# Kernel optimization log

Hardware: AMD Instinct MI355X
Metric: run time of the kernel (lower is better)

Reference implementation:

```python
import jax, jax.numpy as jnp
import numpy as np

N_USERS = 150000
N_ENTITIES = 250000
CH = 64
N_REL = 17
N_FACTORS = 4
N_EDGES = 1_000_000
NNZ = 1_000_000
N_HOPS = 2


def setup_inputs() -> dict:
    key = jax.random.key(0)
    ks = jax.random.split(key, 10)
    user_emb = jax.random.normal(ks[0], (N_USERS, CH), jnp.float32) * 0.1
    entity_emb = jax.random.normal(ks[1], (N_ENTITIES, CH), jnp.float32) * 0.1
    latent_emb = jax.random.normal(ks[2], (N_FACTORS, CH), jnp.float32) * 0.1
    weight = jax.random.normal(ks[3], (N_REL - 1, CH), jnp.float32) * 0.1
    disen_weight_att = jax.random.normal(ks[4], (N_FACTORS, N_REL - 1), jnp.float32) * 0.1
    edge_index = jax.random.randint(ks[5], (2, N_EDGES), 0, N_ENTITIES)
    edge_type = jax.random.randint(ks[6], (N_EDGES,), 1, N_REL)  # in [1, N_REL-1]
    inter_row = jax.random.randint(ks[7], (NNZ,), 0, N_USERS)
    inter_col = jax.random.randint(ks[8], (NNZ,), 0, N_ENTITIES)
    inter_val = jax.random.uniform(ks[9], (NNZ,), jnp.float32)
    return {
        "user_emb": user_emb, "entity_emb": entity_emb, "latent_emb": latent_emb,
        "weight": weight, "disen_weight_att": disen_weight_att, "inter_val": inter_val,
        "edge_index": edge_index, "edge_type": edge_type,
        "inter_row": inter_row, "inter_col": inter_col,
    }


def _l2norm(x):
    # F.normalize(x, dim=1) with eps=1e-12
    n = jnp.linalg.norm(x, axis=1, keepdims=True)
    return x / jnp.maximum(n, 1e-12)


def reference(user_emb, entity_emb, latent_emb, weight, disen_weight_att,
              inter_val, edge_index, edge_type, inter_row, inter_col):
    n_entities = entity_emb.shape[0]
    n_users = user_emb.shape[0]
    head, tail = edge_index[0], edge_index[1]

    # _cul_cor with ind='cosine': sum_{i<j} cos(w_i, w_j)^2 over rows of disen_weight_att
    wn = disen_weight_att / jnp.linalg.norm(disen_weight_att, axis=1, keepdims=True)
    gram = (wn @ wn.T) ** 2  # [F, F]
    cor = jnp.sum(jnp.triu(gram, k=1))

    # constants across hops
    counts = jax.ops.segment_sum(jnp.ones(head.shape[0], jnp.float32), head,
                                 num_segments=n_entities)
    denom = jnp.maximum(counts, 1.0)[:, None]  # scatter_mean denominator (0 -> keep 0)
    disen_weight = jax.nn.softmax(disen_weight_att, axis=-1) @ weight  # [F, C]

    e, u = entity_emb, user_emb
    ent_res, usr_res = entity_emb, user_emb
    for _ in range(N_HOPS):
        # KG aggregate: per-edge gather, relation modulation, scatter_mean into heads
        neigh = e[tail] * weight[edge_type - 1]              # [E, C]
        entity_agg = jax.ops.segment_sum(neigh, head, num_segments=n_entities) / denom

        # user -> latent factor attention
        score = jax.nn.softmax(u @ latent_emb.T, axis=1)[:, :, None]  # [U, F, 1]

        # user aggregate: sparse interact_mat @ entity_emb
        user_agg = jax.ops.segment_sum(inter_val[:, None] * e[inter_col], inter_row,
                                       num_segments=n_users)  # [U, C]
        mix = jnp.sum(disen_weight[None, :, :] * score, axis=1)  # [U, C]
        user_agg = user_agg * mix + user_agg

        e = _l2norm(entity_agg)
        u = _l2norm(user_agg)
        ent_res = ent_res + e
        usr_res = usr_res + u
    return ent_res, usr_res, cor
```

## Files before the change

### kernel.cpp

```cpp
#include <hip/hip_runtime.h>
#include <hip/hip_bf16.h>

#define N_USERS    150000
#define N_ENTITIES 250000
#define CHN        64
#define N_RELM1    16
#define N_FACTORS  4
#define N_EDGES    1000000
#define NNZ_       1000000
#define NRECS      (N_EDGES + NNZ_)

#define BROWS      1024
#define RCAP       8192
#define RCAP_OUT   8192
#define EBUCKETS   245
#define USR0       (EBUCKETS * BROWS)
#define ROWS_EFF   (USR0 + N_USERS)
#define NB         392
#define TILE_A     4096
#define TA_THREADS 512
#define ITEMS_A    8

typedef float vf4 __attribute__((ext_vector_type(4)));

__device__ __forceinline__ unsigned short f2bf(float f) {
    unsigned u = __float_as_uint(f);
    return (unsigned short)((u + 0x7fffu + ((u >> 16) & 1u)) >> 16);
}

__global__ __launch_bounds__(512) void prep_small_kernel(const float* __restrict__ weight,
                                  const float* __restrict__ att,
                                  float* __restrict__ disenw,
                                  float* __restrict__ cor_out,
                                  int* __restrict__ bcur)
{
    int tid = threadIdx.x;
    if (tid < NB) bcur[tid] = tid * RCAP;

    if (tid < 256) {
        int f  = tid >> 6;
        int ch = tid & 63;
        float m = -1e30f;
        for (int r = 0; r < N_RELM1; ++r) m = fmaxf(m, att[f * N_RELM1 + r]);
        float ex[N_RELM1];
        float s = 0.f;
        for (int r = 0; r < N_RELM1; ++r) { ex[r] = expf(att[f * N_RELM1 + r] - m); s += ex[r]; }
        float inv = 1.f / s;
        float acc = 0.f;
        for (int r = 0; r < N_RELM1; ++r) acc += (ex[r] * inv) * weight[r * CHN + ch];
        disenw[f * CHN + ch] = acc;
    }

    if (tid == 0) {
        float wn[N_FACTORS][N_RELM1];
        for (int i = 0; i < N_FACTORS; ++i) {
            float ss = 0.f;
            for (int r = 0; r < N_RELM1; ++r) { float v = att[i * N_RELM1 + r]; ss += v * v; }
            float innv = 1.f / sqrtf(ss);
            for (int r = 0; r < N_RELM1; ++r) wn[i][r] = att[i * N_RELM1 + r] * innv;
        }
        float cor = 0.f;
        for (int i = 0; i < N_FACTORS; ++i)
            for (int j = i + 1; j < N_FACTORS; ++j) {
                float d = 0.f;
                for (int r = 0; r < N_RELM1; ++r) d += wn[i][r] * wn[j][r];
                cor += d * d;
            }
        cor_out[0] = cor;
    }
}

__global__ __launch_bounds__(256) void conv_bf16_kernel(const float4* __restrict__ src,
                                                        ushort4* __restrict__ dst, int n4)
{
    int i = blockIdx.x * 256 + threadIdx.x;
    if (i >= n4) return;
    float4 v = src[i];
    dst[i] = make_ushort4(f2bf(v.x), f2bf(v.y), f2bf(v.z), f2bf(v.w));
}

__global__ __launch_bounds__(TA_THREADS) void bin_pass_kernel(
    const int* __restrict__ head, const int* __restrict__ tail,
    const int* __restrict__ etype, const int* __restrict__ irow,
    const int* __restrict__ icol, const float* __restrict__ val,
    int* __restrict__ bcur, unsigned long long* __restrict__ binned)
{
    __shared__ int cntS[NB], startS[NB], gbase[NB];
    __shared__ unsigned long long buf[TILE_A];
    __shared__ unsigned short bk[TILE_A];

    int tid = threadIdx.x;
    if (tid < NB) cntS[tid] = 0;
    __syncthreads();

    int base = blockIdx.x * TILE_A;
    unsigned long long p[ITEMS_A];
    int bkt[ITEMS_A], rnk[ITEMS_A];
    #pragma unroll
    for (int j = 0; j < ITEMS_A; ++j) {
        int i = base + j * TA_THREADS + tid;
        bkt[j] = -1;
        if (i < NRECS) {
            int row; unsigned long long pay;
            if (i < N_EDGES) {
                row = head[i];
                pay = ((unsigned long long)(unsigned)(etype[i] - 1) << 18) | (unsigned)tail[i];
            } else {
                int jj = i - N_EDGES;
                row = USR0 + irow[jj];
                pay = ((unsigned long long)__float_as_uint(val[jj]) << 18) | (unsigned)icol[jj];
            }
            p[j] = pay | ((unsigned long long)(unsigned)(row & (BROWS - 1)) << 50);
            bkt[j] = row >> 10;
            rnk[j] = atomicAdd(&cntS[bkt[j]], 1);
        }
    }
    __syncthreads();
    if (tid == 0) {
        int s = 0;
        for (int b = 0; b < NB; ++b) { startS[b] = s; s += cntS[b]; }
    }
    __syncthreads();
    if (tid < NB && cntS[tid] > 0) gbase[tid] = atomicAdd(&bcur[tid], cntS[tid]);
    __syncthreads();

    #pragma unroll
    for (int j = 0; j < ITEMS_A; ++j) {
        if (bkt[j] >= 0) {
            int s = startS[bkt[j]] + rnk[j];
            buf[s] = p[j];
            bk[s] = (unsigned short)bkt[j];
        }
    }
    __syncthreads();

    int total = startS[NB - 1] + cntS[NB - 1];
    for (int s = tid; s < total; s += TA_THREADS) {
        int b = bk[s];
        int dst = gbase[b] + (s - startS[b]);
        if (dst < (b + 1) * RCAP) binned[dst] = buf[s];
    }
}

__global__ __launch_bounds__(512) void bucket_scatter_kernel(
    const unsigned long long* __restrict__ binned,
    const int* __restrict__ bcur,
    unsigned int* __restrict__ recsE,
    unsigned long long* __restrict__ recsU,
    int* __restrict__ cnt, int* __restrict__ offs)
{
    __shared__ int rowcnt[BROWS];
    __shared__ int sA[512], sB[512];

    int tid = threadIdx.x;
    int b = blockIdx.x;
    rowcnt[2 * tid] = 0;
    rowcnt[2 * tid + 1] = 0;
    __syncthreads();

    int s0 = b * RCAP;
    int s1 = bcur[b];
    if (s1 > s0 + RCAP) s1 = s0 + RCAP;

    for (int i = s0 + tid; i < s1; i += 512) {
        int rowlo = (int)(binned[i] >> 50) & (BROWS - 1);
        atomicAdd(&rowcnt[rowlo], 1);
    }
    __syncthreads();

    int c0 = rowcnt[2 * tid];
    int c1 = rowcnt[2 * tid + 1];
    int pc0 = (c0 + 1) & ~1;
    int pc1 = (c1 + 1) & ~1;
    sA[tid] = pc0 + pc1;
    __syncthreads();
    int* src = sA; int* dst = sB;
    #pragma unroll
    for (int off = 1; off < 512; off <<= 1) {
        dst[tid] = src[tid] + ((tid >= off) ? src[tid - off] : 0);
        __syncthreads();
        int* tm = src; src = dst; dst = tm;
    }
    int excl = src[tid] - (pc0 + pc1);

    int gbaseOut = (b < EBUCKETS ? b : b - EBUCKETS) * RCAP_OUT;
    int grow = b * BROWS;
    cnt[grow + 2 * tid] = c0;
    offs[grow + 2 * tid] = gbaseOut + excl;
    cnt[grow + 2 * tid + 1] = c1;
    offs[grow + 2 * tid + 1] = gbaseOut + excl + pc0;
    __syncthreads();
    rowcnt[2 * tid] = excl;
    rowcnt[2 * tid + 1] = excl + pc0;
    __syncthreads();

    if (b < EBUCKETS) {
        for (int i = s0 + tid; i < s1; i += 512) {
            unsigned long long p = binned[i];
            int rowlo = (int)(p >> 50) & (BROWS - 1);
            int local = atomicAdd(&rowcnt[rowlo], 1);
            recsE[gbaseOut + local] = (unsigned)(p & ((1ull << 50) - 1));
        }
    } else {
        for (int i = s0 + tid; i < s1; i += 512) {
            unsigned long long p = binned[i];
            int rowlo = (int)(p >> 50) & (BROWS - 1);
            int local = atomicAdd(&rowcnt[rowlo], 1);
            recsU[gbaseOut + local] = p & ((1ull << 50) - 1);
        }
    }
}

__device__ __forceinline__ void fma8w(uint4 g, const float* __restrict__ w, float* acc) {
    acc[0] += __uint_as_float(g.x << 16)          * w[0];
    acc[1] += __uint_as_float(g.x & 0xffff0000u)  * w[1];
    acc[2] += __uint_as_float(g.y << 16)          * w[2];
    acc[3] += __uint_as_float(g.y & 0xffff0000u)  * w[3];
    acc[4] += __uint_as_float(g.z << 16)          * w[4];
    acc[5] += __uint_as_float(g.z & 0xffff0000u)  * w[5];
    acc[6] += __uint_as_float(g.w << 16)          * w[6];
    acc[7] += __uint_as_float(g.w & 0xffff0000u)  * w[7];
}
__device__ __forceinline__ void fma8v(uint4 g, float v, float* acc) {
    acc[0] += __uint_as_float(g.x << 16)          * v;
    acc[1] += __uint_as_float(g.x & 0xffff0000u)  * v;
    acc[2] += __uint_as_float(g.y << 16)          * v;
    acc[3] += __uint_as_float(g.y & 0xffff0000u)  * v;
    acc[4] += __uint_as_float(g.z << 16)          * v;
    acc[5] += __uint_as_float(g.z & 0xffff0000u)  * v;
    acc[6] += __uint_as_float(g.w << 16)          * v;
    acc[7] += __uint_as_float(g.w & 0xffff0000u)  * v;
}

__global__ __launch_bounds__(256) void hop_kernel(const unsigned short* __restrict__ ebf,
                                                  const float* __restrict__ u_src,
                                                  const unsigned int* __restrict__ recsE,
                                                  const unsigned long long* __restrict__ recsU,
                                                  const int* __restrict__ cnt,
                                                  const int* __restrict__ offs,
                                                  const float* __restrict__ weight,
                                                  const float* __restrict__ latent,
                                                  const float* __restrict__ disenw,
                                                  const float* __restrict__ ent_resid,
                                                  const float* __restrict__ usr_resid,
                                                  unsigned short* __restrict__ ebf_new,
                                                  float* __restrict__ u_new,
                                                  float* __restrict__ out_ent,
                                                  float* __restrict__ out_usr)
{
    __shared__ float wl[N_RELM1 * CHN];
    for (int k = threadIdx.x; k < N_RELM1 * CHN; k += 256) wl[k] = weight[k];
    __syncthreads();

    unsigned idx = blockIdx.x * 256u + threadIdx.x;
    unsigned row = idx >> 3;
    int sub = idx & 7;
    int chb = sub * 8;

    float acc[8] = {0.f,0.f,0.f,0.f,0.f,0.f,0.f,0.f};

    if (row < N_ENTITIES) {
        int n = cnt[row];
        int start = offs[row];
        int k = 0;
        for (; k + 4 <= n; k += 4) {
            uint2 ra = *(const uint2*)&recsE[start + k];
            uint2 rb = *(const uint2*)&recsE[start + k + 2];
            uint4 g0 = *(const uint4*)(ebf + (size_t)(ra.x & 0x3FFFF) * CHN + chb);
            uint4 g1 = *(const uint4*)(ebf + (size_t)(ra.y & 0x3FFFF) * CHN + chb);
            uint4 g2 = *(const uint4*)(ebf + (size_t)(rb.x & 0x3FFFF) * CHN + chb);
            uint4 g3 = *(const uint4*)(ebf + (size_t)(rb.y & 0x3FFFF) * CHN + chb);
            fma8w(g0, &wl[(ra.x >> 18) * CHN + chb], acc);
            fma8w(g1, &wl[(ra.y >> 18) * CHN + chb], acc);
            fma8w(g2, &wl[(rb.x >> 18) * CHN + chb], acc);
            fma8w(g3, &wl[(rb.y >> 18) * CHN + chb], acc);
        }
        for (; k < n; ++k) {
            unsigned r0 = recsE[start + k];
            uint4 g0 = *(const uint4*)(ebf + (size_t)(r0 & 0x3FFFF) * CHN + chb);
            fma8w(g0, &wl[(r0 >> 18) * CHN + chb], acc);
        }
        float inv_d = (n > 0) ? (1.f / (float)n) : 1.f;
        float ss = 0.f;
        #pragma unroll
        for (int i = 0; i < 8; ++i) { acc[i] *= inv_d; ss += acc[i] * acc[i]; }
        ss += __shfl_xor(ss, 1, 64);
        ss += __shfl_xor(ss, 2, 64);
        ss += __shfl_xor(ss, 4, 64);
        float innv = 1.f / fmaxf(sqrtf(ss), 1e-12f);
        float y[8];
        #pragma unroll
        for (int i = 0; i < 8; ++i) y[i] = acc[i] * innv;
        if (ebf_new) {
            uint4 pk;
            pk.x = (unsigned)f2bf(y[0]) | ((unsigned)f2bf(y[1]) << 16);
            pk.y = (unsigned)f2bf(y[2]) | ((unsigned)f2bf(y[3]) << 16);
            pk.z = (unsigned)f2bf(y[4]) | ((unsigned)f2bf(y[5]) << 16);
            pk.w = (unsigned)f2bf(y[6]) | ((unsigned)f2bf(y[7]) << 16);
            *(uint4*)(ebf_new + (size_t)row * CHN + chb) = pk;
        }
        const vf4* rp = (const vf4*)&ent_resid[(size_t)row * CHN + chb];
        vf4 r0 = __builtin_nontemporal_load(rp);
        vf4 r1 = __builtin_nontemporal_load(rp + 1);
        vf4* op = (vf4*)&out_ent[(size_t)row * CHN + chb];
        vf4 o0 = {r0.x + y[0], r0.y + y[1], r0.z + y[2], r0.w + y[3]};
        vf4 o1 = {r1.x + y[4], r1.y + y[5], r1.z + y[6], r1.w + y[7]};
        __builtin_nontemporal_store(o0, op);
        __builtin_nontemporal_store(o1, op + 1);
    } else if (row >= USR0 && row < ROWS_EFF) {
        unsigned ur = row - USR0;
        int n = cnt[row];
        int start = offs[row];

        const float4* up = (const float4*)&u_src[(size_t)ur * CHN + chb];
        float4 uo0 = up[0], uo1 = up[1];

        float dotv[N_FACTORS];
        #pragma unroll
        for (int f = 0; f < N_FACTORS; ++f) {
            const float4* lp = (const float4*)&latent[f * CHN + chb];
            float4 l0 = lp[0], l1 = lp[1];
            float p = uo0.x * l0.x + uo0.y * l0.y + uo0.z * l0.z + uo0.w * l0.w
                    + uo1.x * l1.x + uo1.y * l1.y + uo1.z * l1.z + uo1.w * l1.w;
            p += __shfl_xor(p, 1, 64);
            p += __shfl_xor(p, 2, 64);
            p += __shfl_xor(p, 4, 64);
            dotv[f] = p;
        }
        float m = fmaxf(fmaxf(dotv[0], dotv[1]), fmaxf(dotv[2], dotv[3]));
        float es = 0.f;
        #pragma unroll
        for (int f = 0; f < N_FACTORS; ++f) { dotv[f] = expf(dotv[f] - m); es += dotv[f]; }
        float sinv = 1.f / es;
        float mix[8] = {0.f,0.f,0.f,0.f,0.f,0.f,0.f,0.f};
        #pragma unroll
        for (int f = 0; f < N_FACTORS; ++f) {
            float sc = dotv[f] * sinv;
            const float4* dp = (const float4*)&disenw[f * CHN + chb];
            float4 d0 = dp[0], d1 = dp[1];
            mix[0] += sc * d0.x; mix[1] += sc * d0.y; mix[2] += sc * d0.z; mix[3] += sc * d0.w;
            mix[4] += sc * d1.x; mix[5] += sc * d1.y; mix[6] += sc * d1.z; mix[7] += sc * d1.w;
        }

        int k = 0;
        for (; k + 4 <= n; k += 4) {
            ulonglong2 qa = *(const ulonglong2*)&recsU[start + k];
            ulonglong2 qb = *(const ulonglong2*)&recsU[start + k + 2];
            uint4 g0 = *(const uint4*)(ebf + (size_t)(qa.x & 0x3FFFFu) * CHN + chb);
            uint4 g1 = *(const uint4*)(ebf + (size_t)(qa.y & 0x3FFFFu) * CHN + chb);
            uint4 g2 = *(const uint4*)(ebf + (size_t)(qb.x & 0x3FFFFu) * CHN + chb);
            uint4 g3 = *(const uint4*)(ebf + (size_t)(qb.y & 0x3FFFFu) * CHN + chb);
            fma8v(g0, __uint_as_float((unsigned)(qa.x >> 18)), acc);
            fma8v(g1, __uint_as_float((unsigned)(qa.y >> 18)), acc);
            fma8v(g2, __uint_as_float((unsigned)(qb.x >> 18)), acc);
            fma8v(g3, __uint_as_float((unsigned)(qb.y >> 18)), acc);
        }
        for (; k < n; ++k) {
            unsigned long long q0 = recsU[start + k];
            uint4 g0 = *(const uint4*)(ebf + (size_t)(q0 & 0x3FFFFu) * CHN + chb);
            fma8v(g0, __uint_as_float((unsigned)(q0 >> 18)), acc);
        }
        float ss = 0.f;
        #pragma unroll
        for (int i = 0; i < 8; ++i) { acc[i] *= (1.f + mix[i]); ss += acc[i] * acc[i]; }
        ss += __shfl_xor(ss, 1, 64);
        ss += __shfl_xor(ss, 2, 64);
        ss += __shfl_xor(ss, 4, 64);
        float innv = 1.f / fmaxf(sqrtf(ss), 1e-12f);
        float y[8];
        #pragma unroll
        for (int i = 0; i < 8; ++i) y[i] = acc[i] * innv;
        if (u_new) {
            float4* np = (float4*)&u_new[(size_t)ur * CHN + chb];
            np[0] = make_float4(y[0], y[1], y[2], y[3]);
            np[1] = make_float4(y[4], y[5], y[6], y[7]);
        }
        const vf4* rp = (const vf4*)&usr_resid[(size_t)ur * CHN + chb];
        vf4 r0 = __builtin_nontemporal_load(rp);
        vf4 r1 = __builtin_nontemporal_load(rp + 1);
        vf4* op = (vf4*)&out_usr[(size_t)ur * CHN + chb];
        vf4 o0 = {r0.x + y[0], r0.y + y[1], r0.z + y[2], r0.w + y[3]};
        vf4 o1 = {r1.x + y[4], r1.y + y[5], r1.z + y[6], r1.w + y[7]};
        __builtin_nontemporal_store(o0, op);
        __builtin_nontemporal_store(o1, op + 1);
    }
}

extern "C" void kernel_launch(void* const* d_in, const int* in_sizes, int n_in,
                              void* d_out, int out_size, void* d_ws, size_t ws_size,
                              hipStream_t stream) {
    const float* user_emb   = (const float*)d_in[0];
    const float* entity_emb = (const float*)d_in[1];
    const float* latent_emb = (const float*)d_in[2];
    const float* weight     = (const float*)d_in[3];
    const float* att        = (const float*)d_in[4];
    const float* inter_val  = (const float*)d_in[5];
    const int*   edge_index = (const int*)d_in[6];
    const int*   edge_type  = (const int*)d_in[7];
    const int*   inter_row  = (const int*)d_in[8];
    const int*   inter_col  = (const int*)d_in[9];

    const int* head = edge_index;
    const int* tail = edge_index + N_EDGES;

    float* out_ent = (float*)d_out;
    float* out_usr = out_ent + (size_t)N_ENTITIES * CHN;
    float* out_cor = out_usr + (size_t)N_USERS * CHN;

    char* ws = (char*)d_ws;
    unsigned short* ebf0   = (unsigned short*)ws;
    unsigned short* ebfA   = (unsigned short*)(ws + 32000000);
    unsigned long long* binned = (unsigned long long*)(ws + 64000000);
    unsigned long long* recsU  = (unsigned long long*)(ws + 89690112);
    unsigned int* recsE    = (unsigned int*)(ws + 99323904);
    float* u               = (float*)(ws + 107352064);
    float* disenw          = (float*)(ws + 145752064);
    int*   cnt             = (int*)(ws + 145753088);
    int*   offs            = (int*)(ws + 147358720);
    int*   bcur            = (int*)(ws + 148964352);

    prep_small_kernel<<<1, 512, 0, stream>>>(weight, att, disenw, out_cor, bcur);

    {
        int n4 = N_ENTITIES * CHN / 4;
        conv_bf16_kernel<<<(n4 + 255) / 256, 256, 0, stream>>>(
            (const float4*)entity_emb, (ushort4*)ebf0, n4);
    }

    const int binA_blocks = (NRECS + TILE_A - 1) / TILE_A;
    bin_pass_kernel<<<binA_blocks, TA_THREADS, 0, stream>>>(head, tail, edge_type,
                                                            inter_row, inter_col, inter_val,
                                                            bcur, binned);
    bucket_scatter_kernel<<<NB, 512, 0, stream>>>(binned, bcur, recsE, recsU, cnt, offs);

    const int hop_blocks = (ROWS_EFF * 8 + 255) / 256;

    hop_kernel<<<hop_blocks, 256, 0, stream>>>(ebf0, user_emb, recsE, recsU,
                                               cnt, offs, weight, latent_emb, disenw,
                                               entity_emb, user_emb,
                                               ebfA, u, out_ent, out_usr);

    hop_kernel<<<hop_blocks, 256, 0, stream>>>(ebfA, u, recsE, recsU,
                                               cnt, offs, weight, latent_emb, disenw,
                                               out_ent, out_usr,
                                               nullptr, nullptr, out_ent, out_usr);
}
```

Before: 256.6 us.

## Defer residual outputs to second hop, store hop-1 users in bf16, pack cnt/offs

Hop 1 no longer writes the fp32 output residual sums. It only stores the normalized entity and user embeddings in bf16. Hop 2 rebuilds out = emb + hop1 + hop2 by reading the original fp32 embeddings and the bf16 hop-1 values, so one full fp32 read-modify-write of the outputs goes away. The row count and offset are packed into a single 32-bit word, which halves the metadata reads. The cost is reduced precision, since the hop-1 residual and the hop-1 user embedding are now bf16 instead of fp32.

Measured after the change: 227.1 us. 11.5% less time.

```diff
diff --git a/kernel.cpp b/kernel.cpp
--- a/kernel.cpp
+++ b/kernel.cpp
@@ -147,7 +147,7 @@
     const int* __restrict__ bcur,
     unsigned int* __restrict__ recsE,
     unsigned long long* __restrict__ recsU,
-    int* __restrict__ cnt, int* __restrict__ offs)
+    unsigned int* __restrict__ cntoffs)
 {
     __shared__ int rowcnt[BROWS];
     __shared__ int sA[512], sB[512];
@@ -185,10 +185,8 @@
 
     int gbaseOut = (b < EBUCKETS ? b : b - EBUCKETS) * RCAP_OUT;
     int grow = b * BROWS;
-    cnt[grow + 2 * tid] = c0;
-    offs[grow + 2 * tid] = gbaseOut + excl;
-    cnt[grow + 2 * tid + 1] = c1;
-    offs[grow + 2 * tid + 1] = gbaseOut + excl + pc0;
+    cntoffs[grow + 2 * tid]     = ((unsigned)c0 << 22) | (unsigned)(gbaseOut + excl);
+    cntoffs[grow + 2 * tid + 1] = ((unsigned)c1 << 22) | (unsigned)(gbaseOut + excl + pc0);
     __syncthreads();
     rowcnt[2 * tid] = excl;
     rowcnt[2 * tid + 1] = excl + pc0;
@@ -231,22 +229,29 @@
     acc[6] += __uint_as_float(g.w << 16)          * v;
     acc[7] += __uint_as_float(g.w & 0xffff0000u)  * v;
 }
-
-__global__ __launch_bounds__(256) void hop_kernel(const unsigned short* __restrict__ ebf,
-                                                  const float* __restrict__ u_src,
-                                                  const unsigned int* __restrict__ recsE,
-                                                  const unsigned long long* __restrict__ recsU,
-                                                  const int* __restrict__ cnt,
-                                                  const int* __restrict__ offs,
-                                                  const float* __restrict__ weight,
-                                                  const float* __restrict__ latent,
-                                                  const float* __restrict__ disenw,
-                                                  const float* __restrict__ ent_resid,
-                                                  const float* __restrict__ usr_resid,
-                                                  unsigned short* __restrict__ ebf_new,
-                                                  float* __restrict__ u_new,
-                                                  float* __restrict__ out_ent,
-                                                  float* __restrict__ out_usr)
+__device__ __forceinline__ void bf8_unpack(uint4 g, float* o) {
+    o[0] = __uint_as_float(g.x << 16); o[1] = __uint_as_float(g.x & 0xffff0000u);
+    o[2] = __uint_as_float(g.y << 16); o[3] = __uint_as_float(g.y & 0xffff0000u);
+    o[4] = __uint_as_float(g.z << 16); o[5] = __uint_as_float(g.z & 0xffff0000u);
+    o[6] = __uint_as_float(g.w << 16); o[7] = __uint_as_float(g.w & 0xffff0000u);
+}
+
+template<int PASS>
+__global__ __launch_bounds__(256) void hop_kernel(
+    const unsigned short* __restrict__ ebf,
+    const unsigned int* __restrict__ recsE,
+    const unsigned long long* __restrict__ recsU,
+    const unsigned int* __restrict__ cntoffs,
+    const float* __restrict__ weight,
+    const float* __restrict__ latent,
+    const float* __restrict__ disenw,
+    const float* __restrict__ u_emb,
+    const float* __restrict__ e_emb,
+    const unsigned short* __restrict__ ubfA,
+    unsigned short* __restrict__ ebf_new,
+    unsigned short* __restrict__ ubf_new,
+    float* __restrict__ out_ent,
+    float* __restrict__ out_usr)
 {
     __shared__ float wl[N_RELM1 * CHN];
     for (int k = threadIdx.x; k < N_RELM1 * CHN; k += 256) wl[k] = weight[k];
@@ -260,8 +265,9 @@
     float acc[8] = {0.f,0.f,0.f,0.f,0.f,0.f,0.f,0.f};
 
     if (row < N_ENTITIES) {
-        int n = cnt[row];
-        int start = offs[row];
+        unsigned co = cntoffs[row];
+        int n = co >> 22;
+        int start = co & 0x3FFFFF;
         int k = 0;
         for (; k + 4 <= n; k += 4) {
             uint2 ra = *(const uint2*)&recsE[start + k];
@@ -291,37 +297,48 @@
         float y[8];
         #pragma unroll
         for (int i = 0; i < 8; ++i) y[i] = acc[i] * innv;
-        if (ebf_new) {
+        if (PASS == 1) {
             uint4 pk;
             pk.x = (unsigned)f2bf(y[0]) | ((unsigned)f2bf(y[1]) << 16);
             pk.y = (unsigned)f2bf(y[2]) | ((unsigned)f2bf(y[3]) << 16);
             pk.z = (unsigned)f2bf(y[4]) | ((unsigned)f2bf(y[5]) << 16);
             pk.w = (unsigned)f2bf(y[6]) | ((unsigned)f2bf(y[7]) << 16);
             *(uint4*)(ebf_new + (size_t)row * CHN + chb) = pk;
-        }
-        const vf4* rp = (const vf4*)&ent_resid[(size_t)row * CHN + chb];
-        vf4 r0 = __builtin_nontemporal_load(rp);
-        vf4 r1 = __builtin_nontemporal_load(rp + 1);
-        vf4* op = (vf4*)&out_ent[(size_t)row * CHN + chb];
-        vf4 o0 = {r0.x + y[0], r0.y + y[1], r0.z + y[2], r0.w + y[3]};
-        vf4 o1 = {r1.x + y[4], r1.y + y[5], r1.z + y[6], r1.w + y[7]};
-        __builtin_nontemporal_store(o0, op);
-        __builtin_nontemporal_store(o1, op + 1);
+        } else {
+            float y1[8];
+            bf8_unpack(*(const uint4*)(ebf + (size_t)row * CHN + chb), y1);
+            const vf4* bp = (const vf4*)&e_emb[(size_t)row * CHN + chb];
+            vf4 b0 = __builtin_nontemporal_load(bp);
+            vf4 b1 = __builtin_nontemporal_load(bp + 1);
+            vf4* op = (vf4*)&out_ent[(size_t)row * CHN + chb];
+            vf4 o0 = {b0.x + y1[0] + y[0], b0.y + y1[1] + y[1], b0.z + y1[2] + y[2], b0.w + y1[3] + y[3]};
+            vf4 o1 = {b1.x + y1[4] + y[4], b1.y + y1[5] + y[5], b1.z + y1[6] + y[6], b1.w + y1[7] + y[7]};
+            __builtin_nontemporal_store(o0, op);
+            __builtin_nontemporal_store(o1, op + 1);
+        }
     } else if (row >= USR0 && row < ROWS_EFF) {
         unsigned ur = row - USR0;
-        int n = cnt[row];
-        int start = offs[row];
-
-        const float4* up = (const float4*)&u_src[(size_t)ur * CHN + chb];
-        float4 uo0 = up[0], uo1 = up[1];
+        unsigned co = cntoffs[row];
+        int n = co >> 22;
+        int start = co & 0x3FFFFF;
+
+        float uo[8];
+        if (PASS == 1) {
+            const float4* up = (const float4*)&u_emb[(size_t)ur * CHN + chb];
+            float4 a0 = up[0], a1 = up[1];
+            uo[0]=a0.x; uo[1]=a0.y; uo[2]=a0.z; uo[3]=a0.w;
+            uo[4]=a1.x; uo[5]=a1.y; uo[6]=a1.z; uo[7]=a1.w;
+        } else {
+            bf8_unpack(*(const uint4*)(ubfA + (size_t)ur * CHN + chb), uo);
+        }
 
         float dotv[N_FACTORS];
         #pragma unroll
         for (int f = 0; f < N_FACTORS; ++f) {
             const float4* lp = (const float4*)&latent[f * CHN + chb];
             float4 l0 = lp[0], l1 = lp[1];
-            float p = uo0.x * l0.x + uo0.y * l0.y + uo0.z * l0.z + uo0.w * l0.w
-                    + uo1.x * l1.x + uo1.y * l1.y + uo1.z * l1.z + uo1.w * l1.w;
+            float p = uo[0] * l0.x + uo[1] * l0.y + uo[2] * l0.z + uo[3] * l0.w
+                    + uo[4] * l1.x + uo[5] * l1.y + uo[6] * l1.z + uo[7] * l1.w;
             p += __shfl_xor(p, 1, 64);
             p += __shfl_xor(p, 2, 64);
             p += __shfl_xor(p, 4, 64);
@@ -370,19 +387,23 @@
         float y[8];
         #pragma unroll
         for (int i = 0; i < 8; ++i) y[i] = acc[i] * innv;
-        if (u_new) {
-            float4* np = (float4*)&u_new[(size_t)ur * CHN + chb];
-            np[0] = make_float4(y[0], y[1], y[2], y[3]);
-            np[1] = make_float4(y[4], y[5], y[6], y[7]);
-        }
-        const vf4* rp = (const vf4*)&usr_resid[(size_t)ur * CHN + chb];
-        vf4 r0 = __builtin_nontemporal_load(rp);
-        vf4 r1 = __builtin_nontemporal_load(rp + 1);
-        vf4* op = (vf4*)&out_usr[(size_t)ur * CHN + chb];
-        vf4 o0 = {r0.x + y[0], r0.y + y[1], r0.z + y[2], r0.w + y[3]};
-        vf4 o1 = {r1.x + y[4], r1.y + y[5], r1.z + y[6], r1.w + y[7]};
-        __builtin_nontemporal_store(o0, op);
-        __builtin_nontemporal_store(o1, op + 1);
+        if (PASS == 1) {
+            uint4 pk;
+            pk.x = (unsigned)f2bf(y[0]) | ((unsigned)f2bf(y[1]) << 16);
+            pk.y = (unsigned)f2bf(y[2]) | ((unsigned)f2bf(y[3]) << 16);
+            pk.z = (unsigned)f2bf(y[4]) | ((unsigned)f2bf(y[5]) << 16);
+            pk.w = (unsigned)f2bf(y[6]) | ((unsigned)f2bf(y[7]) << 16);
+            *(uint4*)(ubf_new + (size_t)ur * CHN + chb) = pk;
+        } else {
+            const vf4* bp = (const vf4*)&u_emb[(size_t)ur * CHN + chb];
+            vf4 b0 = __builtin_nontemporal_load(bp);
+            vf4 b1 = __builtin_nontemporal_load(bp + 1);
+            vf4* op = (vf4*)&out_usr[(size_t)ur * CHN + chb];
+            vf4 o0 = {b0.x + uo[0] + y[0], b0.y + uo[1] + y[1], b0.z + uo[2] + y[2], b0.w + uo[3] + y[3]};
+            vf4 o1 = {b1.x + uo[4] + y[4], b1.y + uo[5] + y[5], b1.z + uo[6] + y[6], b1.w + uo[7] + y[7]};
+            __builtin_nontemporal_store(o0, op);
+            __builtin_nontemporal_store(o1, op + 1);
+        }
     }
 }
 
@@ -410,14 +431,13 @@
     char* ws = (char*)d_ws;
     unsigned short* ebf0   = (unsigned short*)ws;
     unsigned short* ebfA   = (unsigned short*)(ws + 32000000);
-    unsigned long long* binned = (unsigned long long*)(ws + 64000000);
-    unsigned long long* recsU  = (unsigned long long*)(ws + 89690112);
-    unsigned int* recsE    = (unsigned int*)(ws + 99323904);
-    float* u               = (float*)(ws + 107352064);
-    float* disenw          = (float*)(ws + 145752064);
-    int*   cnt             = (int*)(ws + 145753088);
-    int*   offs            = (int*)(ws + 147358720);
-    int*   bcur            = (int*)(ws + 148964352);
+    unsigned short* ubfA   = (unsigned short*)(ws + 64000000);
+    unsigned long long* binned = (unsigned long long*)(ws + 83200000);
+    unsigned long long* recsU  = (unsigned long long*)(ws + 108890112);
+    unsigned int* recsE    = (unsigned int*)(ws + 118523904);
+    float* disenw          = (float*)(ws + 126552064);
+    unsigned int* cntoffs  = (unsigned int*)(ws + 126553088);
+    int*   bcur            = (int*)(ws + 128158720);
 
     prep_small_kernel<<<1, 512, 0, stream>>>(weight, att, disenw, out_cor, bcur);
 
@@ -431,17 +451,17 @@
     bin_pass_kernel<<<binA_blocks, TA_THREADS, 0, stream>>>(head, tail, edge_type,
                                                             inter_row, inter_col, inter_val,
                                                             bcur, binned);
-    bucket_scatter_kernel<<<NB, 512, 0, stream>>>(binned, bcur, recsE, recsU, cnt, offs);
+    bucket_scatter_kernel<<<NB, 512, 0, stream>>>(binned, bcur, recsE, recsU, cntoffs);
 
     const int hop_blocks = (ROWS_EFF * 8 + 255) / 256;
 
-    hop_kernel<<<hop_blocks, 256, 0, stream>>>(ebf0, user_emb, recsE, recsU,
-                                               cnt, offs, weight, latent_emb, disenw,
-                                               entity_emb, user_emb,
-                                               ebfA, u, out_ent, out_usr);
-
-    hop_kernel<<<hop_blocks, 256, 0, stream>>>(ebfA, u, recsE, recsU,
-                                               cnt, offs, weight, latent_emb, disenw,
-                                               out_ent, out_usr,
-                                               nullptr, nullptr, out_ent, out_usr);
-}
+    hop_kernel<1><<<hop_blocks, 256, 0, stream>>>(ebf0, recsE, recsU, cntoffs,
+                                                  weight, latent_emb, disenw,
+                                                  user_emb, entity_emb, nullptr,
+                                                  ebfA, ubfA, nullptr, nullptr);
+
+    hop_kernel<2><<<hop_blocks, 256, 0, stream>>>(ebfA, recsE, recsU, cntoffs,
+                                                  weight, latent_emb, disenw,
+                                                  user_emb, entity_emb, ubfA,
+                                                  nullptr, nullptr, out_ent, out_usr);
+}
```
